# Optimization experiments

Measured on AMD Instinct MI355X. Metric: run time of the kernel, lower is better.

Reference implementation:

```python
import jax, jax.numpy as jnp
import numpy as np

C = 1.0          # self.c = -curvature = 1.0
SQRT_C = 1.0
EPS = 1e-10
NORM_MAX = 0.99


def setup_inputs() -> dict:
    key = jax.random.key(0)
    k1, k2 = jax.random.split(key)
    b, n, m, d = 4, 4096, 4096, 128
    # scale so points lie inside the Poincare ball (||x|| ~ 0.57 < 1)
    x = jax.random.normal(k1, (b, n, d), dtype=jnp.float32) * 0.05
    y = jax.random.normal(k2, (b, m, d), dtype=jnp.float32) * 0.05
    return {"x": x, "y": y}


def reference(x, y):
    # Pairwise hyperbolic distance d(x_i, y_j) = 2/sqrt(c) * atanh(sqrt(c) * ||(-x_i) (+)_c y_j||)
    # Mobius add: num = A*(-x) + B*y, denom = 1 + 2c<-x,y> + c^2 ||x||^2 ||y||^2
    # with A = 1 + 2c<-x,y> + c||y||^2,  B = 1 - c||x||^2.
    # We never form the (b,n,m,d) tensor: ||A*(-x)+B*y||^2 = A^2||x||^2 - 2AB<x,y> + B^2||y||^2.
    xs = jnp.sum(x * x, axis=-1)                     # (b, n)
    ys = jnp.sum(y * y, axis=-1)                     # (b, m)
    dot = jnp.einsum('bnd,bmd->bnm', x, y)           # (b, n, m) <x_i, y_j>
    xs_ = xs[:, :, None]                             # (b, n, 1)
    ys_ = ys[:, None, :]                             # (b, 1, m)
    A = 1.0 - 2.0 * C * dot + C * ys_                # (b, n, m)
    B = 1.0 - C * xs_                                # (b, n, 1)
    denom = 1.0 - 2.0 * C * dot + (C * C) * xs_ * ys_
    num_sq = A * A * xs_ - 2.0 * A * B * dot + B * B * ys_
    diff_norm = jnp.sqrt(jnp.maximum(num_sq, 0.0)) / jnp.maximum(denom, EPS)
    diff_norm = jnp.clip(diff_norm, EPS, NORM_MAX)
    return (2.0 / SQRT_C) * jnp.arctanh(SQRT_C * diff_norm)
```

## Files before the change

### kernel.cpp

```cpp
#include <hip/hip_runtime.h>
#include <hip/hip_bf16.h>

typedef __bf16 bf16x8 __attribute__((ext_vector_type(8)));
typedef float  f32x4  __attribute__((ext_vector_type(4)));

#define NN 4096
#define DK 128
#define BM 64
#define BN 64
#define NMAX 0.99f
#define LN2F 0.69314718056f

#define WS_XB   0
#define WS_YB   (4u*4096u*DK*2u)
#define WS_XC   (2u*WS_YB)
#define WS_YC   (WS_XC + 4u*4096u*8u)
#define WS_REQ  (WS_YC + 4u*4096u*8u)

__device__ __forceinline__ void load_lds16(const void* g, void* l) {
    __builtin_amdgcn_global_load_lds(
        (const __attribute__((address_space(1))) unsigned int*)g,
        (__attribute__((address_space(3))) unsigned int*)l, 16, 0, 0);
}

__global__ __launch_bounds__(256)
void prep_kernel(const float* __restrict__ X, const float* __restrict__ Y,
                 __bf16* __restrict__ Xb, __bf16* __restrict__ Yb,
                 float2* __restrict__ XC, float2* __restrict__ YC)
{
    const int tid = threadIdx.x;
    const int c16 = tid & 15;
    const int rl  = tid >> 4;
    const int gr  = blockIdx.x * 16 + rl;

    const float* src = blockIdx.y ? Y : X;
    __bf16*      dst = blockIdx.y ? Yb : Xb;
    float2*      nc  = blockIdx.y ? YC : XC;

    const f32x4* s4 = (const f32x4*)(src + (size_t)gr * DK + c16 * 8);
    f32x4 v0 = s4[0], v1 = s4[1];
    float s = v0[0]*v0[0] + v0[1]*v0[1] + v0[2]*v0[2] + v0[3]*v0[3]
            + v1[0]*v1[0] + v1[1]*v1[1] + v1[2]*v1[2] + v1[3]*v1[3];
    s += __shfl_xor(s, 1);
    s += __shfl_xor(s, 2);
    s += __shfl_xor(s, 4);
    s += __shfl_xor(s, 8);

    bf16x8 pk;
    pk[0]=(__bf16)v0[0]; pk[1]=(__bf16)v0[1]; pk[2]=(__bf16)v0[2]; pk[3]=(__bf16)v0[3];
    pk[4]=(__bf16)v1[0]; pk[5]=(__bf16)v1[1]; pk[6]=(__bf16)v1[2]; pk[7]=(__bf16)v1[3];

    const int tile = gr >> 6;
    const int rloc = gr & 63;
    const int byt  = (rloc * 256 + c16 * 16) ^ ((rloc & 7) << 4);
    *(bf16x8*)((char*)(dst + (size_t)tile * (BM * DK)) + byt) = pk;

    if (c16 == 0) nc[gr] = make_float2(s, __logf(1.0f - s));
}

__global__ __launch_bounds__(256, 4)
void hyp_main(const __bf16* __restrict__ Xb, const __bf16* __restrict__ Yb,
              const float2* __restrict__ XC, const float2* __restrict__ YC,
              float* __restrict__ Out)
{
    __shared__ alignas(16) __bf16 aL[BM * DK];
    __shared__ alignas(16) __bf16 bL[BN * DK];
    __shared__ float2 xcL[BM];
    __shared__ float2 ycL[BN];

    const int tid  = threadIdx.x;
    const int lane = tid & 63;
    const int wid  = tid >> 6;
    const int bz   = blockIdx.z;
    const int brow = blockIdx.y * BM;
    const int bcol = blockIdx.x * BN;

    const char* xt = (const char*)(Xb + (size_t)(bz * 64 + blockIdx.y) * (BM * DK));
    const char* yt = (const char*)(Yb + (size_t)(bz * 64 + blockIdx.x) * (BN * DK));

    {
        const int woff = wid * 4096;
#pragma unroll
        for (int j = 0; j < 4; ++j) {
            load_lds16(xt + woff + j * 1024 + lane * 16, (char*)aL + woff + j * 1024);
            load_lds16(yt + woff + j * 1024 + lane * 16, (char*)bL + woff + j * 1024);
        }
    }
    if (tid < 64)        xcL[tid]      = XC[bz * NN + brow + tid];
    else if (tid < 128)  ycL[tid - 64] = YC[bz * NN + bcol + (tid - 64)];
    __syncthreads();

    const int wm  = wid >> 1;
    const int wn  = wid & 1;
    const int r16 = lane & 15;
    const int kg  = lane >> 4;

    bf16x8 bga[4][2];
#pragma unroll
    for (int ks = 0; ks < 4; ++ks) {
        const int kb = ks * 32 + kg * 8;
#pragma unroll
        for (int j = 0; j < 2; ++j) {
            const int r = wn * 32 + j * 16 + r16;
            const int byt = (r * 256 + kb * 2) ^ ((r & 7) << 4);
            bga[ks][j] = *(const bf16x8*)((const char*)bL + byt);
        }
    }

    float* ob = Out + ((size_t)bz * NN + brow) * NN + bcol;

#pragma unroll
    for (int i = 0; i < 2; ++i) {
        f32x4 acc[2] = {};
#pragma unroll
        for (int ks = 0; ks < 4; ++ks) {
            const int kb = ks * 32 + kg * 8;
            const int r  = wm * 32 + i * 16 + r16;
            const int byt = (r * 256 + kb * 2) ^ ((r & 7) << 4);
            const bf16x8 af = *(const bf16x8*)((const char*)aL + byt);
#pragma unroll
            for (int j = 0; j < 2; ++j)
                acc[j] = __builtin_amdgcn_mfma_f32_16x16x32_bf16(bga[ks][j], af, acc[j], 0, 0, 0);
        }

        const int r = wm * 32 + i * 16 + r16;
        const float2 xc = xcL[r];
        const float u = xc.x, cx = xc.y;
        float* orow = ob + (size_t)r * NN;
#pragma unroll
        for (int j = 0; j < 2; ++j) {
            const int cb = wn * 32 + j * 16 + kg * 4;
            const f32x4 y01 = *(const f32x4*)&ycL[cb];
            const f32x4 y23 = *(const f32x4*)&ycL[cb + 2];
            f32x4 o4;
#pragma unroll
            for (int q = 0; q < 4; ++q) {
                const float d  = acc[j][q];
                const float v  = (q < 2) ? y01[2 * q] : y23[2 * (q - 2)];
                const float cy = (q < 2) ? y01[2 * q + 1] : y23[2 * (q - 2) + 1];
                const float e1  = fmaf(-2.0f, d, 1.0f);
                const float den = fmaf(u, v, e1);
                float s = fmaf(-2.0f, d, u + v);
                s = fmaxf(s, 1e-12f);
                const float rt  = __builtin_amdgcn_sqrtf(s * den);
                const float arg = fmaf(2.0f, rt, den + s);
                o4[q] = fmaf(__log2f(arg), LN2F, -(cx + cy));
            }
            *(f32x4*)(orow + cb) = o4;
        }
    }
}

__global__ __launch_bounds__(512, 4)
void hyp_fallback(const float* __restrict__ X, const float* __restrict__ Y,
                  float* __restrict__ Out)
{
    __shared__ alignas(16) __bf16 aL[128 * DK];
    __shared__ alignas(16) __bf16 bL[128 * DK];
    __shared__ float xsL[128];
    __shared__ float ysL[128];

    const int tid  = threadIdx.x;
    const int bz   = blockIdx.z;
    const int brow = blockIdx.y * 128;
    const int bcol = blockIdx.x * 128;
    const float* xb = X + ((size_t)bz * NN + brow) * DK;
    const float* yb = Y + ((size_t)bz * NN + bcol) * DK;
    const int c16 = tid & 15;
    const int rr  = tid >> 4;

#pragma unroll
    for (int p = 0; p < 4; ++p) {
        const int r = p * 32 + rr;
        const f32x4* s4 = (const f32x4*)(xb + r * DK + c16 * 8);
        f32x4 v0 = s4[0], v1 = s4[1];
        float s = v0[0]*v0[0] + v0[1]*v0[1] + v0[2]*v0[2] + v0[3]*v0[3]
                + v1[0]*v1[0] + v1[1]*v1[1] + v1[2]*v1[2] + v1[3]*v1[3];
        s += __shfl_xor(s, 1); s += __shfl_xor(s, 2);
        s += __shfl_xor(s, 4); s += __shfl_xor(s, 8);
        if (c16 == 0) xsL[r] = s;
        bf16x8 pk;
        pk[0]=(__bf16)v0[0]; pk[1]=(__bf16)v0[1]; pk[2]=(__bf16)v0[2]; pk[3]=(__bf16)v0[3];
        pk[4]=(__bf16)v1[0]; pk[5]=(__bf16)v1[1]; pk[6]=(__bf16)v1[2]; pk[7]=(__bf16)v1[3];
        const int byt = (r * 256 + c16 * 16) ^ ((r & 7) << 4);
        *(bf16x8*)((char*)aL + byt) = pk;
    }
#pragma unroll
    for (int p = 0; p < 4; ++p) {
        const int r = p * 32 + rr;
        const f32x4* s4 = (const f32x4*)(yb + r * DK + c16 * 8);
        f32x4 v0 = s4[0], v1 = s4[1];
        float s = v0[0]*v0[0] + v0[1]*v0[1] + v0[2]*v0[2] + v0[3]*v0[3]
                + v1[0]*v1[0] + v1[1]*v1[1] + v1[2]*v1[2] + v1[3]*v1[3];
        s += __shfl_xor(s, 1); s += __shfl_xor(s, 2);
        s += __shfl_xor(s, 4); s += __shfl_xor(s, 8);
        if (c16 == 0) ysL[r] = s;
        bf16x8 pk;
        pk[0]=(__bf16)v0[0]; pk[1]=(__bf16)v0[1]; pk[2]=(__bf16)v0[2]; pk[3]=(__bf16)v0[3];
        pk[4]=(__bf16)v1[0]; pk[5]=(__bf16)v1[1]; pk[6]=(__bf16)v1[2]; pk[7]=(__bf16)v1[3];
        const int byt = (r * 256 + c16 * 16) ^ ((r & 7) << 4);
        *(bf16x8*)((char*)bL + byt) = pk;
    }
    __syncthreads();

    const int lane = tid & 63;
    const int wid  = tid >> 6;
    const int wm   = wid >> 2;
    const int wn   = wid & 3;
    const int r16  = lane & 15;
    const int kg   = lane >> 4;
    f32x4 acc[4][2] = {};
#pragma unroll
    for (int ks = 0; ks < 4; ++ks) {
        const int kb = ks * 32 + kg * 8;
        bf16x8 af[4], bg[2];
#pragma unroll
        for (int i = 0; i < 4; ++i) {
            const int r = wm * 64 + i * 16 + r16;
            const int byt = (r * 256 + kb * 2) ^ ((r & 7) << 4);
            af[i] = *(const bf16x8*)((const char*)aL + byt);
        }
#pragma unroll
        for (int j = 0; j < 2; ++j) {
            const int r = wn * 32 + j * 16 + r16;
            const int byt = (r * 256 + kb * 2) ^ ((r & 7) << 4);
            bg[j] = *(const bf16x8*)((const char*)bL + byt);
        }
#pragma unroll
        for (int i = 0; i < 4; ++i)
#pragma unroll
            for (int j = 0; j < 2; ++j)
                acc[i][j] = __builtin_amdgcn_mfma_f32_16x16x32_bf16(bg[j], af[i], acc[i][j], 0, 0, 0);
    }
    float* ob = Out + ((size_t)bz * NN + brow) * NN + bcol;
#pragma unroll
    for (int i = 0; i < 4; ++i) {
        const int r = wm * 64 + i * 16 + r16;
        const float u = xsL[r];
        float* orow = ob + (size_t)r * NN;
#pragma unroll
        for (int j = 0; j < 2; ++j) {
            const int cb = wn * 32 + j * 16 + kg * 4;
            const f32x4 v4 = *(const f32x4*)&ysL[cb];
            f32x4 o4;
#pragma unroll
            for (int q = 0; q < 4; ++q) {
                const float d  = acc[i][j][q];
                const float v  = v4[q];
                const float e1 = fmaf(-2.0f, d, 1.0f);
                const float den = fmaf(u, v, e1);
                float s = fmaf(-2.0f, d, u + v);
                s = fmaxf(s, 1e-12f);
                const float dn0 = s * __builtin_amdgcn_rsqf(s * den);
                const float dn = fminf(dn0, NMAX);
                o4[q] = __logf((1.0f + dn) * __builtin_amdgcn_rcpf(1.0f - dn));
            }
            *(f32x4*)(orow + cb) = o4;
        }
    }
}

extern "C" void kernel_launch(void* const* d_in, const int* in_sizes, int n_in,
                              void* d_out, int out_size, void* d_ws, size_t ws_size,
                              hipStream_t stream) {
    const float* X = (const float*)d_in[0];
    const float* Y = (const float*)d_in[1];
    float* O = (float*)d_out;
    const int b = in_sizes[0] / (NN * DK);

    if (ws_size >= WS_REQ) {
        __bf16* Xb = (__bf16*)((char*)d_ws + WS_XB);
        __bf16* Yb = (__bf16*)((char*)d_ws + WS_YB);
        float2* XC = (float2*)((char*)d_ws + WS_XC);
        float2* YC = (float2*)((char*)d_ws + WS_YC);
        dim3 pg(b * NN / 16, 2, 1);
        prep_kernel<<<pg, dim3(256), 0, stream>>>(X, Y, Xb, Yb, XC, YC);
        dim3 grid(NN / BN, NN / BM, b);
        hyp_main<<<grid, dim3(256), 0, stream>>>(Xb, Yb, XC, YC, O);
    } else {
        dim3 grid(NN / 128, NN / 128, b);
        hyp_fallback<<<grid, dim3(512), 0, stream>>>(X, Y, O);
    }
}
```

Before: 78.58 us.

## Pre-swizzle inputs into MFMA fragment layout and widen tile to 64x128

The prep kernel now writes bf16 X and Y directly in MFMA fragment order, so each lane's 16-byte operand sits contiguously. The main kernel loads X fragments straight from global memory into registers and stages only Y in LDS, with conflict-free linear LDS reads. The block tile grows to 64 rows by 128 columns, with each wave owning 16 rows across 128 columns, and per-column norms are read directly from global memory instead of LDS. This cuts LDS traffic and address arithmetic per output, in exchange for more accumulator registers and uncached global reads of the Y constants.

```diff
diff --git a/kernel.cpp b/kernel.cpp
--- a/kernel.cpp
+++ b/kernel.cpp
@@ -6,16 +6,14 @@
 
 #define NN 4096
 #define DK 128
-#define BM 64
-#define BN 64
 #define NMAX 0.99f
 #define LN2F 0.69314718056f
 
-#define WS_XB   0
-#define WS_YB   (4u*4096u*DK*2u)
-#define WS_XC   (2u*WS_YB)
-#define WS_YC   (WS_XC + 4u*4096u*8u)
-#define WS_REQ  (WS_YC + 4u*4096u*8u)
+#define WS_XI   0
+#define WS_YI   (4u*NN*DK*2u)
+#define WS_XC   (2u*WS_YI)
+#define WS_YC   (WS_XC + 4u*NN*8u)
+#define WS_REQ  (WS_YC + 4u*NN*8u)
 
 __device__ __forceinline__ void load_lds16(const void* g, void* l) {
     __builtin_amdgcn_global_load_lds(
@@ -25,7 +23,7 @@
 
 __global__ __launch_bounds__(256)
 void prep_kernel(const float* __restrict__ X, const float* __restrict__ Y,
-                 __bf16* __restrict__ Xb, __bf16* __restrict__ Yb,
+                 __bf16* __restrict__ XI, __bf16* __restrict__ YI,
                  float2* __restrict__ XC, float2* __restrict__ YC)
 {
     const int tid = threadIdx.x;
@@ -34,7 +32,7 @@
     const int gr  = blockIdx.x * 16 + rl;
 
     const float* src = blockIdx.y ? Y : X;
-    __bf16*      dst = blockIdx.y ? Yb : Xb;
+    __bf16*      dst = blockIdx.y ? YI : XI;
     float2*      nc  = blockIdx.y ? YC : XC;
 
     const f32x4* s4 = (const f32x4*)(src + (size_t)gr * DK + c16 * 8);
@@ -50,104 +48,86 @@
     pk[0]=(__bf16)v0[0]; pk[1]=(__bf16)v0[1]; pk[2]=(__bf16)v0[2]; pk[3]=(__bf16)v0[3];
     pk[4]=(__bf16)v1[0]; pk[5]=(__bf16)v1[1]; pk[6]=(__bf16)v1[2]; pk[7]=(__bf16)v1[3];
 
-    const int tile = gr >> 6;
-    const int rloc = gr & 63;
-    const int byt  = (rloc * 256 + c16 * 16) ^ ((rloc & 7) << 4);
-    *(bf16x8*)((char*)(dst + (size_t)tile * (BM * DK)) + byt) = pk;
+    const int bz = gr >> 12;
+    const int gl = gr & (NN - 1);
+    const int ks = c16 >> 2, kg = c16 & 3;
+    char* img = (char*)dst + (size_t)bz * (NN * DK * 2);
+    const int off = (((gl >> 4) * 4 + ks) << 10) + kg * 256 + (gl & 15) * 16;
+    *(bf16x8*)(img + off) = pk;
 
     if (c16 == 0) nc[gr] = make_float2(s, __logf(1.0f - s));
 }
 
 __global__ __launch_bounds__(256, 4)
-void hyp_main(const __bf16* __restrict__ Xb, const __bf16* __restrict__ Yb,
+void hyp_main(const __bf16* __restrict__ XI, const __bf16* __restrict__ YI,
               const float2* __restrict__ XC, const float2* __restrict__ YC,
               float* __restrict__ Out)
 {
-    __shared__ alignas(16) __bf16 aL[BM * DK];
-    __shared__ alignas(16) __bf16 bL[BN * DK];
-    __shared__ float2 xcL[BM];
-    __shared__ float2 ycL[BN];
+    __shared__ alignas(16) char bL[32 * 1024];
 
     const int tid  = threadIdx.x;
     const int lane = tid & 63;
-    const int wid  = tid >> 6;
+    const int w    = tid >> 6;
     const int bz   = blockIdx.z;
-    const int brow = blockIdx.y * BM;
-    const int bcol = blockIdx.x * BN;
-
-    const char* xt = (const char*)(Xb + (size_t)(bz * 64 + blockIdx.y) * (BM * DK));
-    const char* yt = (const char*)(Yb + (size_t)(bz * 64 + blockIdx.x) * (BN * DK));
+    const int brow = blockIdx.x * 64;
+    const int bcol = blockIdx.y * 128;
+
+    const char* ximg = (const char*)XI + (size_t)bz * (NN * DK * 2);
+    const char* yimg = (const char*)YI + (size_t)bz * (NN * DK * 2) + ((bcol >> 4) << 12);
 
     {
-        const int woff = wid * 4096;
-#pragma unroll
-        for (int j = 0; j < 4; ++j) {
-            load_lds16(xt + woff + j * 1024 + lane * 16, (char*)aL + woff + j * 1024);
-            load_lds16(yt + woff + j * 1024 + lane * 16, (char*)bL + woff + j * 1024);
-        }
-    }
-    if (tid < 64)        xcL[tid]      = XC[bz * NN + brow + tid];
-    else if (tid < 128)  ycL[tid - 64] = YC[bz * NN + bcol + (tid - 64)];
-    __syncthreads();
-
-    const int wm  = wid >> 1;
-    const int wn  = wid & 1;
+        const int woff = w * 8192;
+#pragma unroll
+        for (int p = 0; p < 8; ++p)
+            load_lds16(yimg + woff + p * 1024 + lane * 16, bL + woff + p * 1024);
+    }
+
+    const int xrb = (brow >> 4) + w;
+    bf16x8 af[4];
+#pragma unroll
+    for (int ks = 0; ks < 4; ++ks)
+        af[ks] = *(const bf16x8*)(ximg + (((xrb * 4 + ks) << 10) + lane * 16));
+
     const int r16 = lane & 15;
     const int kg  = lane >> 4;
-
-    bf16x8 bga[4][2];
+    const int orow_idx = brow + w * 16 + r16;
+    const float2 xc = XC[bz * NN + orow_idx];
+
+    __syncthreads();
+
+    f32x4 acc[8] = {};
 #pragma unroll
     for (int ks = 0; ks < 4; ++ks) {
-        const int kb = ks * 32 + kg * 8;
-#pragma unroll
-        for (int j = 0; j < 2; ++j) {
-            const int r = wn * 32 + j * 16 + r16;
-            const int byt = (r * 256 + kb * 2) ^ ((r & 7) << 4);
-            bga[ks][j] = *(const bf16x8*)((const char*)bL + byt);
-        }
-    }
-
-    float* ob = Out + ((size_t)bz * NN + brow) * NN + bcol;
-
-#pragma unroll
-    for (int i = 0; i < 2; ++i) {
-        f32x4 acc[2] = {};
-#pragma unroll
-        for (int ks = 0; ks < 4; ++ks) {
-            const int kb = ks * 32 + kg * 8;
-            const int r  = wm * 32 + i * 16 + r16;
-            const int byt = (r * 256 + kb * 2) ^ ((r & 7) << 4);
-            const bf16x8 af = *(const bf16x8*)((const char*)aL + byt);
-#pragma unroll
-            for (int j = 0; j < 2; ++j)
-                acc[j] = __builtin_amdgcn_mfma_f32_16x16x32_bf16(bga[ks][j], af, acc[j], 0, 0, 0);
-        }
-
-        const int r = wm * 32 + i * 16 + r16;
-        const float2 xc = xcL[r];
-        const float u = xc.x, cx = xc.y;
-        float* orow = ob + (size_t)r * NN;
-#pragma unroll
-        for (int j = 0; j < 2; ++j) {
-            const int cb = wn * 32 + j * 16 + kg * 4;
-            const f32x4 y01 = *(const f32x4*)&ycL[cb];
-            const f32x4 y23 = *(const f32x4*)&ycL[cb + 2];
-            f32x4 o4;
-#pragma unroll
-            for (int q = 0; q < 4; ++q) {
-                const float d  = acc[j][q];
-                const float v  = (q < 2) ? y01[2 * q] : y23[2 * (q - 2)];
-                const float cy = (q < 2) ? y01[2 * q + 1] : y23[2 * (q - 2) + 1];
-                const float e1  = fmaf(-2.0f, d, 1.0f);
-                const float den = fmaf(u, v, e1);
-                float s = fmaf(-2.0f, d, u + v);
-                s = fmaxf(s, 1e-12f);
-                const float rt  = __builtin_amdgcn_sqrtf(s * den);
-                const float arg = fmaf(2.0f, rt, den + s);
-                o4[q] = fmaf(__log2f(arg), LN2F, -(cx + cy));
-            }
-            *(f32x4*)(orow + cb) = o4;
-        }
+#pragma unroll
+        for (int j = 0; j < 8; ++j) {
+            const bf16x8 bg = *(const bf16x8*)(bL + (((j * 4 + ks) << 10) + lane * 16));
+            acc[j] = __builtin_amdgcn_mfma_f32_16x16x32_bf16(bg, af[ks], acc[j], 0, 0, 0);
+        }
+    }
+
+    const float u = xc.x, cx = xc.y;
+    float* orow = Out + ((size_t)bz * NN + orow_idx) * NN + bcol;
+    const float2* YCb = YC + bz * NN + bcol;
+#pragma unroll
+    for (int j = 0; j < 8; ++j) {
+        const int cb = j * 16 + kg * 4;
+        const f32x4 y01 = *(const f32x4*)(YCb + cb);
+        const f32x4 y23 = *(const f32x4*)(YCb + cb + 2);
+        f32x4 o4;
+#pragma unroll
+        for (int q = 0; q < 4; ++q) {
+            const float d  = acc[j][q];
+            const float v  = (q < 2) ? y01[2 * q] : y23[2 * (q - 2)];
+            const float cy = (q < 2) ? y01[2 * q + 1] : y23[2 * (q - 2) + 1];
+            const float e1  = fmaf(-2.0f, d, 1.0f);
+            const float den = fmaf(u, v, e1);
+            float s = fmaf(-2.0f, d, u + v);
+            s = fmaxf(s, 1e-12f);
+            const float rt  = __builtin_amdgcn_sqrtf(s * den);
+            const float arg = fmaf(2.0f, rt, den + s);
+            o4[q] = fmaf(__log2f(arg), LN2F, -(cx + cy));
+        }
+        *(f32x4*)(orow + cb) = o4;
     }
 }
 
@@ -269,14 +249,14 @@
     const int b = in_sizes[0] / (NN * DK);
 
     if (ws_size >= WS_REQ) {
-        __bf16* Xb = (__bf16*)((char*)d_ws + WS_XB);
-        __bf16* Yb = (__bf16*)((char*)d_ws + WS_YB);
+        __bf16* XI = (__bf16*)((char*)d_ws + WS_XI);
+        __bf16* YI = (__bf16*)((char*)d_ws + WS_YI);
         float2* XC = (float2*)((char*)d_ws + WS_XC);
         float2* YC = (float2*)((char*)d_ws + WS_YC);
         dim3 pg(b * NN / 16, 2, 1);
-        prep_kernel<<<pg, dim3(256), 0, stream>>>(X, Y, Xb, Yb, XC, YC);
-        dim3 grid(NN / BN, NN / BM, b);
-        hyp_main<<<grid, dim3(256), 0, stream>>>(Xb, Yb, XC, YC, O);
+        prep_kernel<<<pg, dim3(256), 0, stream>>>(X, Y, XI, YI, XC, YC);
+        dim3 grid(NN / 64, NN / 128, b);
+        hyp_main<<<grid, dim3(256), 0, stream>>>(XI, YI, XC, YC, O);
     } else {
         dim3 grid(NN / 128, NN / 128, b);
         hyp_fallback<<<grid, dim3(512), 0, stream>>>(X, Y, O);
```

Measured after the change: 85.78 us. 9.2% more time.
